# Optimization experiments

Measured on AMD Instinct MI355X. Metric: run time of the kernel, lower is better.

Reference implementation:

```python
import jax, jax.numpy as jnp
import numpy as np

B, NS, NT, C = 32, 1000, 100, 256
LAMBDA_GIOU, LAMBDA_L1 = 10.0, 1.0


def _lsa(cost):
    """Hungarian / Jonker-Volgenant shortest-augmenting-path (numpy, O(n^2 m)).
    Matches scipy.optimize.linear_sum_assignment for rectangular matrices."""
    cost = np.asarray(cost, dtype=np.float64)
    transposed = cost.shape[0] > cost.shape[1]
    if transposed:
        cost = cost.T
    n, m = cost.shape  # n <= m
    INF = np.inf
    u = np.zeros(n + 1)
    v = np.zeros(m + 1)
    p = np.zeros(m + 1, dtype=np.int64)   # p[j] = row (1-based) assigned to col j
    way = np.zeros(m + 1, dtype=np.int64)
    for i in range(1, n + 1):
        p[0] = i
        j0 = 0
        minv = np.full(m + 1, INF)
        used = np.zeros(m + 1, dtype=bool)
        while True:
            used[j0] = True
            i0 = p[j0]
            cur = cost[i0 - 1, :] - u[i0] - v[1:]
            free = ~used[1:]
            better = free & (cur < minv[1:])
            minv[1:][better] = cur[better]
            way[1:][better] = j0
            masked = np.where(free, minv[1:], INF)
            j1 = int(np.argmin(masked)) + 1
            delta = masked[j1 - 1]
            u[p[used]] += delta
            v[used] -= delta
            minv[~used] -= delta
            j0 = j1
            if p[j0] == 0:
                break
        while j0:
            j1 = way[j0]
            p[j0] = p[j1]
            j0 = j1
    rows = p[1:] - 1
    cols = np.arange(m)
    keep = rows >= 0
    rows, cols = rows[keep], cols[keep]
    if transposed:
        rows, cols = cols, rows
    order = np.argsort(rows)
    return rows[order], cols[order]


def _pairwise_cost(logits, classes, sb, tb):
    """Per-batch (Ns,Nt) cost = CE(logits_s, class_t) + 10*(1-GIoU(box_s, box_t)) + L1mean."""
    Bc, Ns, Cd = logits.shape
    Nt = classes.shape[1]
    # Cross entropy: logsumexp over classes minus logit at target class (identical
    # math to the torch expand+flatten CE, without the Ns*Nt*C copy).
    lse = jax.nn.logsumexp(logits, axis=-1)  # (B,Ns)
    picked = jnp.take_along_axis(
        logits, jnp.broadcast_to(classes[:, None, :], (Bc, Ns, Nt)), axis=2)  # (B,Ns,Nt)
    ce = lse[:, :, None] - picked
    # Pairwise GIoU (boxes in xyxy)
    s = sb[:, :, None, :]  # (B,Ns,1,4)
    t = tb[:, None, :, :]  # (B,1,Nt,4)
    ix1 = jnp.maximum(s[..., 0], t[..., 0])
    iy1 = jnp.maximum(s[..., 1], t[..., 1])
    ix2 = jnp.minimum(s[..., 2], t[..., 2])
    iy2 = jnp.minimum(s[..., 3], t[..., 3])
    inter = jnp.clip(ix2 - ix1, 0.0) * jnp.clip(iy2 - iy1, 0.0)
    area_s = (s[..., 2] - s[..., 0]) * (s[..., 3] - s[..., 1])
    area_t = (t[..., 2] - t[..., 0]) * (t[..., 3] - t[..., 1])
    union = area_s + area_t - inter
    iou = inter / union
    cx1 = jnp.minimum(s[..., 0], t[..., 0])
    cy1 = jnp.minimum(s[..., 1], t[..., 1])
    cx2 = jnp.maximum(s[..., 2], t[..., 2])
    cy2 = jnp.maximum(s[..., 3], t[..., 3])
    carea = (cx2 - cx1) * (cy2 - cy1)
    giou = iou - (carea - union) / carea
    l1 = jnp.abs(s - t).mean(axis=-1)  # (B,Ns,Nt)
    return ce + LAMBDA_GIOU * (1.0 - giou) + LAMBDA_L1 * l1


def _valid_boxes(key, b, n):
    p = jax.random.uniform(key, (b, n, 2, 2), dtype=jnp.float32)
    lo = p.min(axis=2)
    hi = p.max(axis=2)
    return jnp.concatenate([lo, hi], axis=-1)  # (b,n,4) xyxy, x1<x2, y1<y2


def setup_inputs() -> dict:
    key = jax.random.key(0)
    k1, k2, k3, k4 = jax.random.split(key, 4)
    return {
        "source_class_logits": jax.random.normal(k1, (B, NS, C), dtype=jnp.float32),
        "target_classes": jax.random.randint(k2, (B, NT), 0, C, dtype=jnp.int32),
        "source_boxes": _valid_boxes(k3, B, NS),
        "target_boxes": _valid_boxes(k4, B, NT),
    }


def reference(source_class_logits, target_classes, source_boxes, target_boxes):
    cost = _pairwise_cost(source_class_logits, target_classes, source_boxes, target_boxes)
    cost_np = np.asarray(cost)
    rows_l, cols_l = [], []
    for b in range(cost_np.shape[0]):  # assignment is inherently per-matrix / host-side
        r, c = _lsa(cost_np[b])
        rows_l.append(r)
        cols_l.append(c)
    rows = jnp.asarray(np.stack(rows_l))  # (B, min(Ns,Nt))
    cols = jnp.asarray(np.stack(cols_l))
    bidx = jnp.arange(cost.shape[0])[:, None]
    return cost[bidx, rows, cols].mean(axis=1)  # (B,)
```

## Files before the change

kernel.cpp:

```cpp
#include <hip/hip_runtime.h>
#include <math.h>

#define NSRC 1000
#define NTGT 100
#define NCLS 256
#define NB   32
#define NSP  1024
#define PAD_IDX(j) ((j) + ((j) >> 4))
#define LDSN (NSP + (NSP >> 4))

__global__ __launch_bounds__(256) void lse_kernel(const float* __restrict__ logits,
                                                  float* __restrict__ lse) {
    int wid  = threadIdx.x >> 6;
    int lane = threadIdx.x & 63;
    int row0 = blockIdx.x * 32 + wid * 8;
    #pragma unroll 2
    for (int r = 0; r < 8; ++r) {
        int row = row0 + r;
        float4 v4 = reinterpret_cast<const float4*>(logits + (size_t)row * NCLS)[lane];
        float m = fmaxf(fmaxf(v4.x, v4.y), fmaxf(v4.z, v4.w));
        #pragma unroll
        for (int off = 32; off >= 1; off >>= 1) m = fmaxf(m, __shfl_xor(m, off));
        float s = expf(v4.x - m) + expf(v4.y - m) + expf(v4.z - m) + expf(v4.w - m);
        #pragma unroll
        for (int off = 32; off >= 1; off >>= 1) s += __shfl_xor(s, off);
        if (lane == 0) lse[row] = m + logf(s);
    }
}

__global__ __launch_bounds__(256) void cost_kernel(const float* __restrict__ logits,
                                                   const int*   __restrict__ tcls,
                                                   const float* __restrict__ sbox,
                                                   const float* __restrict__ tbox,
                                                   const float* __restrict__ lse,
                                                   float*       __restrict__ cost,
                                                   float*       __restrict__ urow_g,
                                                   int*         __restrict__ jmin_g) {
    int b  = blockIdx.x & 31;
    int t  = blockIdx.x >> 5;
    int bt = b * NTGT + t;
    int cls = tcls[bt];
    float4 tb = reinterpret_cast<const float4*>(tbox)[bt];
    float area_t = (tb.z - tb.x) * (tb.w - tb.y);
    float* crow = cost + (size_t)bt * NSP;
    float m = 1e38f; int mi = 0x7fffffff;
    for (int s = threadIdx.x; s < NSP; s += 256) {
        if (s >= NSRC) { crow[s] = 1e30f; continue; }
        int gs = b * NSRC + s;
        float4 sb = reinterpret_cast<const float4*>(sbox)[gs];
        float ce = lse[gs] - logits[(size_t)gs * NCLS + cls];
        float ix1 = fmaxf(sb.x, tb.x), iy1 = fmaxf(sb.y, tb.y);
        float ix2 = fminf(sb.z, tb.z), iy2 = fminf(sb.w, tb.w);
        float inter = fmaxf(ix2 - ix1, 0.f) * fmaxf(iy2 - iy1, 0.f);
        float area_s = (sb.z - sb.x) * (sb.w - sb.y);
        float uni = area_s + area_t - inter;
        float iou = inter / uni;
        float cx1 = fminf(sb.x, tb.x), cy1 = fminf(sb.y, tb.y);
        float cx2 = fmaxf(sb.z, tb.z), cy2 = fmaxf(sb.w, tb.w);
        float carea = (cx2 - cx1) * (cy2 - cy1);
        float giou = iou - (carea - uni) / carea;
        float l1 = 0.25f * (fabsf(sb.x - tb.x) + fabsf(sb.y - tb.y) +
                            fabsf(sb.z - tb.z) + fabsf(sb.w - tb.w));
        float c = ce + 10.0f * (1.0f - giou) + l1;
        crow[s] = c;
        if (c < m) { m = c; mi = s; }
    }
    #pragma unroll
    for (int off = 32; off >= 1; off >>= 1) {
        float om = __shfl_xor(m, off);
        int   oi = __shfl_xor(mi, off);
        if (om < m || (om == m && oi < mi)) { m = om; mi = oi; }
    }
    __shared__ float smin[4];
    __shared__ int   sidx[4];
    int wid = threadIdx.x >> 6, lane = threadIdx.x & 63;
    if (lane == 0) { smin[wid] = m; sidx[wid] = mi; }
    __syncthreads();
    if (threadIdx.x == 0) {
        #pragma unroll
        for (int w = 1; w < 4; ++w) {
            float om = smin[w]; int oi = sidx[w];
            if (om < m || (om == m && oi < mi)) { m = om; mi = oi; }
        }
        urow_g[bt] = m;
        jmin_g[bt] = mi;
    }
}

__global__ __launch_bounds__(64) void lsa_kernel(const float* __restrict__ cost,
                                                 const float* __restrict__ urow_g,
                                                 const int*   __restrict__ jmin_g,
                                                 float* __restrict__ out) {
    int b    = blockIdx.x;
    int lane = threadIdx.x;
    const float* C = cost + (size_t)b * NTGT * NSP;
    __shared__ int   way[LDSN];
    __shared__ int   pcol[LDSN];
    __shared__ float uu[LDSN];
    __shared__ float urow[NTGT];
    __shared__ int   jmin[NTGT];
    __shared__ int   done[NTGT];
    __shared__ int   queue[512];
    for (int t = lane; t < LDSN; t += 64) { pcol[t] = -1; uu[t] = 0.f; way[t] = 0x7fffffff; }
    for (int t = lane; t < NTGT; t += 64) {
        urow[t] = urow_g[b * NTGT + t];
        jmin[t] = jmin_g[b * NTGT + t];
    }
    float v[16], d[16];
    #pragma unroll
    for (int k = 0; k < 16; ++k) v[k] = 0.f;
    int base = lane * 16;
    __syncthreads();

    for (int r = lane; r < NTGT; r += 64) atomicMin(&way[PAD_IDX(jmin[r])], r);
    __syncthreads();
    for (int r = lane; r < NTGT; r += 64) {
        int j = jmin[r];
        int w = (way[PAD_IDX(j)] == r) ? 1 : 0;
        done[r] = w;
        if (w) { pcol[PAD_IDX(j)] = r; uu[PAD_IDX(j)] = urow[r]; }
    }
    __syncthreads();

    int qh = 0, qt = 0;
    for (int r = 0; r < NTGT; ++r) {
        if (!done[r]) { if (lane == 0) queue[qt] = r; qt++; }
    }
    __syncthreads();
    int steps = 0;
    while (qh < qt && steps < 400) {
        ++steps;
        int i = queue[qh++];
        const float4* row4 = reinterpret_cast<const float4*>(C + (size_t)i * NSP + base);
        float m1 = 1e38f, m2 = 1e38f; int j1 = 0x7fffffff;
        #pragma unroll
        for (int q = 0; q < 4; ++q) {
            float4 c4 = row4[q];
            float vals[4] = {c4.x - v[4*q+0], c4.y - v[4*q+1],
                             c4.z - v[4*q+2], c4.w - v[4*q+3]};
            #pragma unroll
            for (int e = 0; e < 4; ++e) {
                float val = vals[e];
                if (val < m1) { m2 = m1; m1 = val; j1 = base + 4*q + e; }
                else m2 = fminf(m2, val);
            }
        }
        #pragma unroll
        for (int off = 32; off >= 1; off >>= 1) {
            float om1 = __shfl_xor(m1, off);
            float om2 = __shfl_xor(m2, off);
            int   oj1 = __shfl_xor(j1, off);
            bool take = (om1 < m1) || (om1 == m1 && oj1 < j1);
            float lose = take ? m1 : om1;
            m1 = take ? om1 : m1;
            j1 = take ? oj1 : j1;
            m2 = fminf(fminf(m2, om2), lose);
        }
        int old = pcol[PAD_IDX(j1)];
        if ((j1 >> 4) == lane) v[j1 & 15] -= (m2 - m1);
        if (lane == 0) {
            pcol[PAD_IDX(j1)] = i;
            uu[PAD_IDX(j1)]   = m2;
            urow[i] = m2;
            done[i] = 1;
            if (old >= 0) { queue[qt] = old; done[old] = 0; }
        }
        if (old >= 0) qt++;
        __syncthreads();
    }
    __syncthreads();

    for (int i = 0; i < NTGT; ++i) {
        if (done[i]) continue;
        float ui = urow[i];
        {
            const float4* row4 = reinterpret_cast<const float4*>(C + (size_t)i * NSP + base);
            #pragma unroll
            for (int q = 0; q < 4; ++q) {
                float4 c4 = row4[q];
                d[4*q+0] = c4.x - ui - v[4*q+0];
                d[4*q+1] = c4.y - ui - v[4*q+1];
                d[4*q+2] = c4.z - ui - v[4*q+2];
                d[4*q+3] = c4.w - ui - v[4*q+3];
            }
        }
        #pragma unroll
        for (int k = 0; k < 16; ++k) way[PAD_IDX(base + k)] = -1;
        unsigned int used = 0;
        float Df = 0.f;
        int jf = -1;

        for (int it = 0; it < NTGT + 3; ++it) {
            float lmin = 1e38f;
            #pragma unroll
            for (int k = 0; k < 16; ++k) {
                float val = ((used >> k) & 1u) ? 1e38f : d[k];
                lmin = fminf(lmin, val);
            }
            float wmin = lmin;
            #pragma unroll
            for (int off = 32; off >= 1; off >>= 1) wmin = fminf(wmin, __shfl_xor(wmin, off));
            unsigned long long msk = __ballot(lmin == wmin);
            int src = __ffsll(msk) - 1;
            int myk = -1;
            #pragma unroll
            for (int k = 15; k >= 0; --k)
                if (!((used >> k) & 1u) && d[k] == wmin) myk = k;
            int j0 = __shfl(base + myk, src);
            if (j0 < 0) break;
            int pj0 = pcol[PAD_IDX(j0)];
            if (pj0 < 0) { Df = wmin; jf = j0; break; }
            if ((j0 >> 4) == lane) used |= 1u << (j0 & 15);
            float uref = uu[PAD_IDX(j0)];
            float sft  = wmin - uref;
            const float4* rr = reinterpret_cast<const float4*>(C + (size_t)pj0 * NSP + base);
            float cr[16];
            #pragma unroll
            for (int q = 0; q < 4; ++q) {
                float4 c4 = rr[q];
                cr[4*q+0] = c4.x; cr[4*q+1] = c4.y; cr[4*q+2] = c4.z; cr[4*q+3] = c4.w;
            }
            #pragma unroll
            for (int k = 0; k < 16; ++k) {
                float cand = sft + cr[k] - v[k];
                bool upd = (cand < d[k]) && !((used >> k) & 1u);
                if (upd) { d[k] = cand; way[PAD_IDX(base + k)] = j0; }
            }
        }

        if (jf >= 0) {
            #pragma unroll
            for (int k = 0; k < 16; ++k) {
                if ((used >> k) & 1u) {
                    float diff = Df - d[k];
                    v[k] -= diff;
                    uu[PAD_IDX(base + k)] += diff;
                }
            }
        }
        __syncthreads();
        if (lane == 0 && jf >= 0) {
            int j = jf;
            for (int g = 0; g < NSP; ++g) {
                int jp = way[PAD_IDX(j)];
                if (jp < 0) { pcol[PAD_IDX(j)] = i; uu[PAD_IDX(j)] = ui + Df; break; }
                pcol[PAD_IDX(j)] = pcol[PAD_IDX(jp)];
                uu[PAD_IDX(j)]   = uu[PAD_IDX(jp)];
                j = jp;
            }
            done[i] = 1;
        }
        __syncthreads();
    }

    float acc = 0.f;
    #pragma unroll
    for (int k = 0; k < 16; ++k) {
        int j = base + k;
        if (j < NSRC) {
            int r = pcol[PAD_IDX(j)];
            if (r >= 0) acc += C[(size_t)r * NSP + j];
        }
    }
    #pragma unroll
    for (int off = 32; off >= 1; off >>= 1) acc += __shfl_xor(acc, off);
    if (lane == 0) out[b] = acc * (1.0f / NTGT);
}

extern "C" void kernel_launch(void* const* d_in, const int* in_sizes, int n_in,
                              void* d_out, int out_size, void* d_ws, size_t ws_size,
                              hipStream_t stream) {
    const float* logits = (const float*)d_in[0];
    const int*   tcls   = (const int*)  d_in[1];
    const float* sbox   = (const float*)d_in[2];
    const float* tbox   = (const float*)d_in[3];
    float* out = (float*)d_out;

    float* lse    = (float*)d_ws;
    float* cost   = lse + 32768;
    float* urow_g = cost + (size_t)NB * NTGT * NSP;
    int*   jmin_g = (int*)(urow_g + NB * NTGT);

    lse_kernel <<<1000,      256, 0, stream>>>(logits, lse);
    cost_kernel<<<NB * NTGT, 256, 0, stream>>>(logits, tcls, sbox, tbox, lse, cost,
                                               urow_g, jmin_g);
    lsa_kernel <<<NB,        64,  0, stream>>>(cost, urow_g, jmin_g, out);
}
```

Baseline: 153.8 us.

## Add epsilon auction bidding with precomputed second-min to skip initial row scans

The cost kernel now also records each row's second-smallest cost, so the first bid of each unassigned row in the auction phase can reuse the precomputed min and second-min instead of rescanning the row from global memory, provided the chosen column's price is still zero. Bid increments are clamped to a minimum epsilon, which bounds how many price wars occur before the later exact phase. Queue setup now uses a ballot-based parallel compaction. Column prices are mirrored into shared memory to check whether a shortcut is valid, which adds a write and some register-indexing work per step.

```diff
diff --git a/kernel.cpp b/kernel.cpp
--- a/kernel.cpp
+++ b/kernel.cpp
@@ -8,6 +8,7 @@
 #define NSP  1024
 #define PAD_IDX(j) ((j) + ((j) >> 4))
 #define LDSN (NSP + (NSP >> 4))
+#define AUCTION_EPS 0.01f
 
 __global__ __launch_bounds__(256) void lse_kernel(const float* __restrict__ logits,
                                                   float* __restrict__ lse) {
@@ -35,7 +36,8 @@
                                                    const float* __restrict__ lse,
                                                    float*       __restrict__ cost,
                                                    float*       __restrict__ urow_g,
-                                                   int*         __restrict__ jmin_g) {
+                                                   int*         __restrict__ jmin_g,
+                                                   float*       __restrict__ m2_g) {
     int b  = blockIdx.x & 31;
     int t  = blockIdx.x >> 5;
     int bt = b * NTGT + t;
@@ -43,7 +45,7 @@
     float4 tb = reinterpret_cast<const float4*>(tbox)[bt];
     float area_t = (tb.z - tb.x) * (tb.w - tb.y);
     float* crow = cost + (size_t)bt * NSP;
-    float m = 1e38f; int mi = 0x7fffffff;
+    float m1 = 1e38f, m2 = 1e38f; int mi = 0x7fffffff;
     for (int s = threadIdx.x; s < NSP; s += 256) {
         if (s >= NSRC) { crow[s] = 1e30f; continue; }
         int gs = b * NSRC + s;
@@ -63,33 +65,45 @@
                             fabsf(sb.z - tb.z) + fabsf(sb.w - tb.w));
         float c = ce + 10.0f * (1.0f - giou) + l1;
         crow[s] = c;
-        if (c < m) { m = c; mi = s; }
+        if (c < m1) { m2 = m1; m1 = c; mi = s; }
+        else if (c < m2) m2 = c;
     }
     #pragma unroll
     for (int off = 32; off >= 1; off >>= 1) {
-        float om = __shfl_xor(m, off);
-        int   oi = __shfl_xor(mi, off);
-        if (om < m || (om == m && oi < mi)) { m = om; mi = oi; }
-    }
-    __shared__ float smin[4];
+        float om1 = __shfl_xor(m1, off);
+        float om2 = __shfl_xor(m2, off);
+        int   oi  = __shfl_xor(mi, off);
+        bool take = (om1 < m1) || (om1 == m1 && oi < mi);
+        float lose = take ? m1 : om1;
+        m1 = take ? om1 : m1;
+        mi = take ? oi  : mi;
+        m2 = fminf(fminf(m2, om2), lose);
+    }
+    __shared__ float smin[4], smin2[4];
     __shared__ int   sidx[4];
     int wid = threadIdx.x >> 6, lane = threadIdx.x & 63;
-    if (lane == 0) { smin[wid] = m; sidx[wid] = mi; }
+    if (lane == 0) { smin[wid] = m1; smin2[wid] = m2; sidx[wid] = mi; }
     __syncthreads();
     if (threadIdx.x == 0) {
         #pragma unroll
         for (int w = 1; w < 4; ++w) {
-            float om = smin[w]; int oi = sidx[w];
-            if (om < m || (om == m && oi < mi)) { m = om; mi = oi; }
-        }
-        urow_g[bt] = m;
+            float om1 = smin[w], om2 = smin2[w]; int oi = sidx[w];
+            bool take = (om1 < m1) || (om1 == m1 && oi < mi);
+            float lose = take ? m1 : om1;
+            m1 = take ? om1 : m1;
+            mi = take ? oi  : mi;
+            m2 = fminf(fminf(m2, om2), lose);
+        }
+        urow_g[bt] = m1;
         jmin_g[bt] = mi;
+        m2_g[bt]   = m2;
     }
 }
 
 __global__ __launch_bounds__(64) void lsa_kernel(const float* __restrict__ cost,
                                                  const float* __restrict__ urow_g,
                                                  const int*   __restrict__ jmin_g,
+                                                 const float* __restrict__ m2_g,
                                                  float* __restrict__ out) {
     int b    = blockIdx.x;
     int lane = threadIdx.x;
@@ -97,14 +111,19 @@
     __shared__ int   way[LDSN];
     __shared__ int   pcol[LDSN];
     __shared__ float uu[LDSN];
+    __shared__ float vsh[LDSN];
     __shared__ float urow[NTGT];
+    __shared__ float m2s[NTGT];
     __shared__ int   jmin[NTGT];
     __shared__ int   done[NTGT];
-    __shared__ int   queue[512];
-    for (int t = lane; t < LDSN; t += 64) { pcol[t] = -1; uu[t] = 0.f; way[t] = 0x7fffffff; }
+    __shared__ int   queue[768];
+    for (int t = lane; t < LDSN; t += 64) {
+        pcol[t] = -1; uu[t] = 0.f; vsh[t] = 0.f; way[t] = 0x7fffffff;
+    }
     for (int t = lane; t < NTGT; t += 64) {
         urow[t] = urow_g[b * NTGT + t];
         jmin[t] = jmin_g[b * NTGT + t];
+        m2s[t]  = m2_g[b * NTGT + t];
     }
     float v[16], d[16];
     #pragma unroll
@@ -122,46 +141,67 @@
     }
     __syncthreads();
 
-    int qh = 0, qt = 0;
-    for (int r = 0; r < NTGT; ++r) {
-        if (!done[r]) { if (lane == 0) queue[qt] = r; qt++; }
-    }
-    __syncthreads();
-    int steps = 0;
-    while (qh < qt && steps < 400) {
+    int qt = 0;
+    #pragma unroll
+    for (int r0 = 0; r0 < 128; r0 += 64) {
+        int r = r0 + lane;
+        bool act = (r < NTGT) && !done[r];
+        unsigned long long mask = __ballot(act);
+        if (act) queue[qt + __popcll(mask & ((1ull << lane) - 1ull))] = r;
+        qt += __popcll(mask);
+    }
+    int qinit = qt;
+    __syncthreads();
+
+    int qh = 0, steps = 0;
+    while (qh < qt && steps < 600) {
         ++steps;
-        int i = queue[qh++];
-        const float4* row4 = reinterpret_cast<const float4*>(C + (size_t)i * NSP + base);
-        float m1 = 1e38f, m2 = 1e38f; int j1 = 0x7fffffff;
-        #pragma unroll
-        for (int q = 0; q < 4; ++q) {
-            float4 c4 = row4[q];
-            float vals[4] = {c4.x - v[4*q+0], c4.y - v[4*q+1],
-                             c4.z - v[4*q+2], c4.w - v[4*q+3]};
-            #pragma unroll
-            for (int e = 0; e < 4; ++e) {
-                float val = vals[e];
-                if (val < m1) { m2 = m1; m1 = val; j1 = base + 4*q + e; }
-                else m2 = fminf(m2, val);
-            }
-        }
-        #pragma unroll
-        for (int off = 32; off >= 1; off >>= 1) {
-            float om1 = __shfl_xor(m1, off);
-            float om2 = __shfl_xor(m2, off);
-            int   oj1 = __shfl_xor(j1, off);
-            bool take = (om1 < m1) || (om1 == m1 && oj1 < j1);
-            float lose = take ? m1 : om1;
-            m1 = take ? om1 : m1;
-            j1 = take ? oj1 : j1;
-            m2 = fminf(fminf(m2, om2), lose);
-        }
+        int  i      = queue[qh];
+        bool isInit = (qh < qinit);
+        ++qh;
+        int j1; float m1, m2;
+        int   pj  = jmin[i];
+        float vpj = vsh[PAD_IDX(pj)];
+        if (isInit && vpj == 0.0f) {
+            j1 = pj; m1 = urow[i]; m2 = m2s[i];
+        } else {
+            const float4* row4 = reinterpret_cast<const float4*>(C + (size_t)i * NSP + base);
+            m1 = 1e38f; m2 = 1e38f; j1 = 0x7fffffff;
+            #pragma unroll
+            for (int q = 0; q < 4; ++q) {
+                float4 c4 = row4[q];
+                float vals[4] = {c4.x - v[4*q+0], c4.y - v[4*q+1],
+                                 c4.z - v[4*q+2], c4.w - v[4*q+3]};
+                #pragma unroll
+                for (int e = 0; e < 4; ++e) {
+                    float val = vals[e];
+                    if (val < m1) { m2 = m1; m1 = val; j1 = base + 4*q + e; }
+                    else m2 = fminf(m2, val);
+                }
+            }
+            #pragma unroll
+            for (int off = 32; off >= 1; off >>= 1) {
+                float om1 = __shfl_xor(m1, off);
+                float om2 = __shfl_xor(m2, off);
+                int   oj1 = __shfl_xor(j1, off);
+                bool take = (om1 < m1) || (om1 == m1 && oj1 < j1);
+                float lose = take ? m1 : om1;
+                m1 = take ? om1 : m1;
+                j1 = take ? oj1 : j1;
+                m2 = fminf(fminf(m2, om2), lose);
+            }
+        }
+        float delta = fmaxf(m2 - m1, AUCTION_EPS);
         int old = pcol[PAD_IDX(j1)];
-        if ((j1 >> 4) == lane) v[j1 & 15] -= (m2 - m1);
+        if ((j1 >> 4) == lane) {
+            #pragma unroll
+            for (int k = 0; k < 16; ++k)
+                if ((j1 & 15) == k) { v[k] -= delta; vsh[PAD_IDX(j1)] = v[k]; }
+        }
         if (lane == 0) {
             pcol[PAD_IDX(j1)] = i;
-            uu[PAD_IDX(j1)]   = m2;
-            urow[i] = m2;
+            uu[PAD_IDX(j1)]   = m1 + delta;
+            urow[i] = m1 + delta;
             done[i] = 1;
             if (old >= 0) { queue[qt] = old; done[old] = 0; }
         }
@@ -280,9 +320,10 @@
     float* cost   = lse + 32768;
     float* urow_g = cost + (size_t)NB * NTGT * NSP;
     int*   jmin_g = (int*)(urow_g + NB * NTGT);
+    float* m2_g   = (float*)(jmin_g + NB * NTGT);
 
     lse_kernel <<<1000,      256, 0, stream>>>(logits, lse);
     cost_kernel<<<NB * NTGT, 256, 0, stream>>>(logits, tcls, sbox, tbox, lse, cost,
-                                               urow_g, jmin_g);
-    lsa_kernel <<<NB,        64,  0, stream>>>(cost, urow_g, jmin_g, out);
+                                               urow_g, jmin_g, m2_g);
+    lsa_kernel <<<NB,        64,  0, stream>>>(cost, urow_g, jmin_g, m2_g, out);
 }
```

New measurement: 150.7 us. 1.02x faster.
